# Kernel optimization log

Measured on AMD Instinct MI355X. Metric: run time of the kernel, lower is better.

## Reference

```python
import jax, jax.numpy as jnp
import numpy as np

HIDDEN = 64
EPS = 0.001


def _gru_cell(x, h, w_ih, w_hh, b_ih, b_hh):
    # PyTorch GRUCell math. w_ih: [3H, D], w_hh: [3H, H], gates ordered (r, z, n).
    gi = x @ w_ih.T + b_ih  # [B, 3H]
    gh = h @ w_hh.T + b_hh  # [B, 3H]
    i_r, i_z, i_n = jnp.split(gi, 3, axis=-1)
    h_r, h_z, h_n = jnp.split(gh, 3, axis=-1)
    r = jax.nn.sigmoid(i_r + h_r)
    z = jax.nn.sigmoid(i_z + h_z)
    n = jnp.tanh(i_n + r * h_n)
    return (1.0 - z) * n + z * h


def setup_inputs() -> dict:
    key = jax.random.key(0)
    ks = jax.random.split(key, 12)
    B, T, state_dim, action_dim = 2048, 512, 64, 8
    H = HIDDEN
    k_in = 1.0 / np.sqrt(H)  # PyTorch GRUCell init bound
    u = lambda k, shp: jax.random.uniform(k, shp, jnp.float32, -k_in, k_in)
    return {
        "state": jax.random.normal(ks[0], (B, T, state_dim), jnp.float32),
        "w_ih1": u(ks[1], (3 * H, state_dim)),
        "w_hh1": u(ks[2], (3 * H, H)),
        "b_ih1": u(ks[3], (3 * H,)),
        "b_hh1": u(ks[4], (3 * H,)),
        "w_ih2": u(ks[5], (3 * H, H)),
        "w_hh2": u(ks[6], (3 * H, H)),
        "b_ih2": u(ks[7], (3 * H,)),
        "b_hh2": u(ks[8], (3 * H,)),
        "fc_w": jax.random.uniform(ks[9], (action_dim, H), jnp.float32, -EPS, EPS),
        "fc_b": u(ks[10], (action_dim,)),
    }


def reference(state, w_ih1, w_hh1, b_ih1, b_hh1, w_ih2, w_hh2, b_ih2, b_hh2, fc_w, fc_b):
    B = state.shape[0]
    h0 = jnp.zeros((B, HIDDEN), state.dtype)

    def step(carry, x_t):
        s1, s2 = carry
        s1 = _gru_cell(x_t, s1, w_ih1, w_hh1, b_ih1, b_hh1)
        s2 = _gru_cell(s1, s2, w_ih2, w_hh2, b_ih2, b_hh2)
        return (s1, s2), None

    xs = jnp.swapaxes(state, 0, 1)  # [T, B, state_dim]
    (_, s2), _ = jax.lax.scan(step, (h0, h0), xs)
    return s2 @ fc_w.T + fc_b  # [B, action_dim]
```

## Files before the change

### kernel.cpp

```cpp
#include <hip/hip_runtime.h>

#define T_STEPS 512
#define HID 64
#define SPB 8
#define NT 512

typedef _Float16 f16x8 __attribute__((ext_vector_type(8)));
typedef float f32x4 __attribute__((ext_vector_type(4)));

#define MFMA(a, b, c) __builtin_amdgcn_mfma_f32_16x16x32_f16(a, b, c, 0, 0, 0)

#define LOG2E 1.44269504088896340736f

__device__ __forceinline__ unsigned pkh(float a, float b) {
    unsigned short ua = __builtin_bit_cast(unsigned short, (_Float16)a);
    unsigned short ub = __builtin_bit_cast(unsigned short, (_Float16)b);
    return (unsigned)ua | ((unsigned)ub << 16);
}
__device__ __forceinline__ float dpp_ror8(float x) {
    int i = __builtin_bit_cast(int, x);
    int r = __builtin_amdgcn_mov_dpp(i, 0x128, 0xF, 0xF, true);
    return __builtin_bit_cast(float, r);
}
__device__ __forceinline__ char* swz(const void* base, int s, int kbyte) {
    int off = s * 128 + kbyte;
    off ^= (s & 7) << 4;
    return (char*)base + off;
}
__device__ __forceinline__ f16x8 g8rowS(const float* __restrict__ p, float s) {
    f16x8 r;
#pragma unroll
    for (int j = 0; j < 8; ++j) r[j] = (_Float16)(p[j] * s);
    return r;
}

#define BAR() do { asm volatile("s_waitcnt lgkmcnt(0)" ::: "memory"); \
                   __builtin_amdgcn_s_barrier();                      \
                   asm volatile("" ::: "memory"); } while (0)

__global__ __launch_bounds__(NT, 1)
void gru2_pf2(const float* __restrict__ state,
              const float* __restrict__ w_ih1, const float* __restrict__ w_hh1,
              const float* __restrict__ b_ih1, const float* __restrict__ b_hh1,
              const float* __restrict__ w_ih2, const float* __restrict__ w_hh2,
              const float* __restrict__ b_ih2, const float* __restrict__ b_hh2,
              const float* __restrict__ fc_w,  const float* __restrict__ fc_b,
              float* __restrict__ out)
{
    __shared__ __align__(16) unsigned short xb[2][16][64];
    __shared__ __align__(16) unsigned short h1b[2][16][64];
    __shared__ __align__(16) unsigned short h2b[2][16][64];

    const int tid  = threadIdx.x;
    const int wv8  = tid >> 6;
    const bool isA = wv8 < 4;
    const int w    = wv8 & 3;
    const int lane = tid & 63;
    const int i16  = lane & 15;
    const int g    = lane >> 4;
    const int g8   = g * 8;
    const int b0   = blockIdx.x * SPB;
    const bool realc = (i16 < 8);

    const float* Wp = isA ? w_ih1 : w_ih2;
    const float* Wq = isA ? w_hh1 : w_hh2;
    const float* Bi = isA ? b_ih1 : b_ih2;
    const float* Bh = isA ? b_hh1 : b_hh2;

    const int rA = (16 * w + i16) * HID;
    const int zA = rA + 64 * HID;
    const int nA = rA + 128 * HID;
    f16x8 ar[4], az[4], ani[2], anh[2];
    ar[0]  = g8rowS(Wp + rA + g8, -LOG2E);  ar[1]  = g8rowS(Wp + rA + 32 + g8, -LOG2E);
    ar[2]  = g8rowS(Wq + rA + g8, -LOG2E);  ar[3]  = g8rowS(Wq + rA + 32 + g8, -LOG2E);
    az[0]  = g8rowS(Wp + zA + g8, -LOG2E);  az[1]  = g8rowS(Wp + zA + 32 + g8, -LOG2E);
    az[2]  = g8rowS(Wq + zA + g8, -LOG2E);  az[3]  = g8rowS(Wq + zA + 32 + g8, -LOG2E);
    ani[0] = g8rowS(Wp + nA + g8, 2.0f * LOG2E);
    ani[1] = g8rowS(Wp + nA + 32 + g8, 2.0f * LOG2E);
    anh[0] = g8rowS(Wq + nA + g8, 2.0f * LOG2E);
    anh[1] = g8rowS(Wq + nA + 32 + g8, 2.0f * LOG2E);

    f32x4 bR4, bZ4, bNi4, bNh4;
#pragma unroll
    for (int q = 0; q < 4; ++q) {
        const int r0 = 16 * w + 4 * g + q;
        bR4[q]  = -LOG2E * (Bi[r0] + Bh[r0]);
        bZ4[q]  = -LOG2E * (Bi[64 + r0] + Bh[64 + r0]);
        bNi4[q] = 2.0f * LOG2E * Bi[128 + r0];
        bNh4[q] = 2.0f * LOG2E * Bh[128 + r0];
    }

    char* rp[2][2]; char* rq[2][2]; char* wd[2]; char* sa[2];
    const int scol = i16 & 7;
    const int qb4  = realc ? 0 : 4;
#pragma unroll
    for (int c = 0; c < 2; ++c) {
        const void* Pb = isA ? (const void*)xb[c]      : (const void*)h1b[c ^ 1];
        const void* Qb = isA ? (const void*)h1b[c ^ 1] : (const void*)h2b[c];
        void* Db       = isA ? (void*)h1b[c]           : (void*)h2b[c ^ 1];
        rp[c][0] = swz(Pb, i16, 16 * g);
        rp[c][1] = swz(Pb, i16, 64 + 16 * g);
        rq[c][0] = swz(Qb, i16, 16 * g);
        rq[c][1] = swz(Qb, i16, 64 + 16 * g);
        wd[c]    = swz(Db, scol, 32 * w + 8 * g + qb4);
        sa[c]    = swz(xb[c ^ 1], (tid >> 5) & 7, (tid & 31) * 4);
    }

    for (int k = tid; k < 2 * 16 * 64; k += NT) {
        ((unsigned short*)xb)[k]  = 0;
        ((unsigned short*)h1b)[k] = 0;
        ((unsigned short*)h2b)[k] = 0;
    }
    __syncthreads();

    const int ss = (tid >> 5) & 7;
    const int sk = (tid & 31) * 2;
    const float* xgp = state + (size_t)(b0 + ss) * T_STEPS * HID + sk;
    float2 PFa = make_float2(0.0f, 0.0f);
    float2 PFb = make_float2(0.0f, 0.0f);
    if (tid < 256) {
        float2 v0 = *(const float2*)xgp;
        *(unsigned*)swz(xb[0], ss, sk * 2) = pkh(v0.x, v0.y);
        PFa = *(const float2*)(xgp + HID);
        PFb = *(const float2*)(xgp + 2 * HID);
    }
    const float* xnext = xgp + 3 * HID;
    __syncthreads();

    float hr0 = 0.0f, hr1 = 0.0f;
    f16x8 p0 = {}, p1 = {}, q0 = {}, q1 = {};

#define ITER(TT, CUR)                                                            \
  {                                                                              \
    const bool active = isA ? ((TT) < T_STEPS) : ((TT) >= 1);                    \
    if (active) {                                                                \
      if (realc) {       \
        p0 = *(const f16x8*)rp[CUR][0];                                          \
        p1 = *(const f16x8*)rp[CUR][1];                                          \
        q0 = *(const f16x8*)rq[CUR][0];                                          \
        q1 = *(const f16x8*)rq[CUR][1];                                          \
      }                                                                          \
      __builtin_amdgcn_s_setprio(1);                                             \
      f32x4 aR  = MFMA(ar[0], p0, bR4);                                          \
      f32x4 aZ  = MFMA(az[0], p0, bZ4);                                          \
      f32x4 aNi = MFMA(ani[0], p0, bNi4);                                        \
      f32x4 aNh = MFMA(anh[0], q0, bNh4);                                        \
      aR  = MFMA(ar[1], p1, aR);   aR  = MFMA(ar[2], q0, aR);                    \
      aR  = MFMA(ar[3], q1, aR);                                                 \
      aZ  = MFMA(az[1], p1, aZ);   aZ  = MFMA(az[2], q0, aZ);                    \
      aZ  = MFMA(az[3], q1, aZ);                                                 \
      aNi = MFMA(ani[1], p1, aNi);                                               \
      aNh = MFMA(anh[1], q1, aNh);                                               \
      __builtin_amdgcn_s_setprio(0);                                             \
        \
      float vR0  = realc ? aR[0]  : dpp_ror8(aR[2]);                             \
      float vR1  = realc ? aR[1]  : dpp_ror8(aR[3]);                             \
      float vZ0  = realc ? aZ[0]  : dpp_ror8(aZ[2]);                             \
      float vZ1  = realc ? aZ[1]  : dpp_ror8(aZ[3]);                             \
      float vNi0 = realc ? aNi[0] : dpp_ror8(aNi[2]);                            \
      float vNi1 = realc ? aNi[1] : dpp_ror8(aNi[3]);                            \
      float vNh0 = realc ? aNh[0] : dpp_ror8(aNh[2]);                            \
      float vNh1 = realc ? aNh[1] : dpp_ror8(aNh[3]);                            \
      {                                                                          \
        float rg0 = __builtin_amdgcn_rcpf(1.0f + __builtin_amdgcn_exp2f(vR0));   \
        float zg0 = __builtin_amdgcn_rcpf(1.0f + __builtin_amdgcn_exp2f(vZ0));   \
        float e20 = __builtin_amdgcn_exp2f(fmaf(rg0, vNh0, vNi0));               \
        float ng0 = fmaf(-2.0f, __builtin_amdgcn_rcpf(1.0f + e20), 1.0f);        \
        hr0 = fmaf(zg0, hr0 - ng0, ng0);                                         \
        float rg1 = __builtin_amdgcn_rcpf(1.0f + __builtin_amdgcn_exp2f(vR1));   \
        float zg1 = __builtin_amdgcn_rcpf(1.0f + __builtin_amdgcn_exp2f(vZ1));   \
        float e21 = __builtin_amdgcn_exp2f(fmaf(rg1, vNh1, vNi1));               \
        float ng1 = fmaf(-2.0f, __builtin_amdgcn_rcpf(1.0f + e21), 1.0f);        \
        hr1 = fmaf(zg1, hr1 - ng1, ng1);                                         \
      }                                                                          \
      *(unsigned*)wd[CUR] = pkh(hr0, hr1);                                       \
    }                                                                            \
    if (tid < 256 && (TT) < T_STEPS) {                                           \
      *(unsigned*)sa[CUR] = pkh(PFa.x, PFa.y);   \
      PFa = PFb;                                                                 \
      PFb = *(const float2*)xnext;                            \
      xnext += ((TT) <= T_STEPS - 5) ? HID : 0;                                  \
    }                                                                            \
    BAR();                                                                       \
  }

    for (int t = 0; t < T_STEPS; t += 2) {
        ITER(t, 0)
        ITER(t + 1, 1)
    }
    ITER(T_STEPS, 0)
#undef ITER

    if (tid < 64) {
        const int s = tid >> 3, a = tid & 7;
        float acc = fc_b[a];
#pragma unroll
        for (int j = 0; j < HID; ++j) {
            _Float16 hv = *(_Float16*)swz(h2b[1], s, j * 2);
            acc = fmaf((float)hv, fc_w[a * HID + j], acc);
        }
        out[(size_t)(b0 + s) * 8 + a] = acc;
    }
}

extern "C" void kernel_launch(void* const* d_in, const int* in_sizes, int n_in,
                              void* d_out, int out_size, void* d_ws, size_t ws_size,
                              hipStream_t stream) {
    (void)in_sizes; (void)n_in; (void)d_ws; (void)ws_size; (void)out_size;
    const float* state = (const float*)d_in[0];
    const float* w_ih1 = (const float*)d_in[1];
    const float* w_hh1 = (const float*)d_in[2];
    const float* b_ih1 = (const float*)d_in[3];
    const float* b_hh1 = (const float*)d_in[4];
    const float* w_ih2 = (const float*)d_in[5];
    const float* w_hh2 = (const float*)d_in[6];
    const float* b_ih2 = (const float*)d_in[7];
    const float* b_hh2 = (const float*)d_in[8];
    const float* fc_w  = (const float*)d_in[9];
    const float* fc_b  = (const float*)d_in[10];
    float* out = (float*)d_out;

    dim3 grid(2048 / SPB);
    dim3 block(NT);
    gru2_pf2<<<grid, block, 0, stream>>>(state,
                                         w_ih1, w_hh1, b_ih1, b_hh1,
                                         w_ih2, w_hh2, b_ih2, b_hh2,
                                         fc_w, fc_b, out);
}
```

Measured before the change: 242.3 us.

## Stagger GRU layer phases so MFMA and gate math of the two layers alternate

Splits each timestep into two barrier-separated halves. Layer-1 waves run their MFMAs while layer-2 waves run gate activations, and then the roles swap. The goal is to spread matrix-core and transcendental/VALU work evenly across the phases instead of having every wave contend for the same unit at once. In exchange it doubles the barriers per step and changes the h2 double-buffer indexing, so correctness depends on the new buffer parity and lag.

```diff
diff --git a/kernel.cpp b/kernel.cpp
--- a/kernel.cpp
+++ b/kernel.cpp
@@ -38,14 +38,59 @@
                    __builtin_amdgcn_s_barrier();                      \
                    asm volatile("" ::: "memory"); } while (0)
 
+#define GATES_WRITE(CUR)                                                       \
+  {                                                                            \
+    float vR0  = realc ? aR[0]  : dpp_ror8(aR[2]);                             \
+    float vR1  = realc ? aR[1]  : dpp_ror8(aR[3]);                             \
+    float vZ0  = realc ? aZ[0]  : dpp_ror8(aZ[2]);                             \
+    float vZ1  = realc ? aZ[1]  : dpp_ror8(aZ[3]);                             \
+    float vNi0 = realc ? aNi[0] : dpp_ror8(aNi[2]);                            \
+    float vNi1 = realc ? aNi[1] : dpp_ror8(aNi[3]);                            \
+    float vNh0 = realc ? aNh[0] : dpp_ror8(aNh[2]);                            \
+    float vNh1 = realc ? aNh[1] : dpp_ror8(aNh[3]);                            \
+    float rg0 = __builtin_amdgcn_rcpf(1.0f + __builtin_amdgcn_exp2f(vR0));     \
+    float zg0 = __builtin_amdgcn_rcpf(1.0f + __builtin_amdgcn_exp2f(vZ0));     \
+    float e20 = __builtin_amdgcn_exp2f(fmaf(rg0, vNh0, vNi0));                 \
+    float ng0 = fmaf(-2.0f, __builtin_amdgcn_rcpf(1.0f + e20), 1.0f);          \
+    hr0 = fmaf(zg0, hr0 - ng0, ng0);                                           \
+    float rg1 = __builtin_amdgcn_rcpf(1.0f + __builtin_amdgcn_exp2f(vR1));     \
+    float zg1 = __builtin_amdgcn_rcpf(1.0f + __builtin_amdgcn_exp2f(vZ1));     \
+    float e21 = __builtin_amdgcn_exp2f(fmaf(rg1, vNh1, vNi1));                 \
+    float ng1 = fmaf(-2.0f, __builtin_amdgcn_rcpf(1.0f + e21), 1.0f);          \
+    hr1 = fmaf(zg1, hr1 - ng1, ng1);                                           \
+    *(unsigned*)wd[CUR] = pkh(hr0, hr1);                                       \
+  }
+
+#define READ_MFMA(CUR)                                                         \
+  {                                                                            \
+    if (realc) {                                                               \
+      p0 = *(const f16x8*)rp[CUR][0];                                          \
+      p1 = *(const f16x8*)rp[CUR][1];                                          \
+      q0 = *(const f16x8*)rq[CUR][0];                                          \
+      q1 = *(const f16x8*)rq[CUR][1];                                          \
+    }                                                                          \
+    __builtin_amdgcn_s_setprio(1);                                             \
+    aR  = MFMA(ar[0], p0, bR4);                                                \
+    aZ  = MFMA(az[0], p0, bZ4);                                                \
+    aNi = MFMA(ani[0], p0, bNi4);                                              \
+    aNh = MFMA(anh[0], q0, bNh4);                                              \
+    aR  = MFMA(ar[1], p1, aR);   aR  = MFMA(ar[2], q0, aR);                    \
+    aR  = MFMA(ar[3], q1, aR);                                                 \
+    aZ  = MFMA(az[1], p1, aZ);   aZ  = MFMA(az[2], q0, aZ);                    \
+    aZ  = MFMA(az[3], q1, aZ);                                                 \
+    aNi = MFMA(ani[1], p1, aNi);                                               \
+    aNh = MFMA(anh[1], q1, aNh);                                               \
+    __builtin_amdgcn_s_setprio(0);                                             \
+  }
+
 __global__ __launch_bounds__(NT, 1)
-void gru2_pf2(const float* __restrict__ state,
-              const float* __restrict__ w_ih1, const float* __restrict__ w_hh1,
-              const float* __restrict__ b_ih1, const float* __restrict__ b_hh1,
-              const float* __restrict__ w_ih2, const float* __restrict__ w_hh2,
-              const float* __restrict__ b_ih2, const float* __restrict__ b_hh2,
-              const float* __restrict__ fc_w,  const float* __restrict__ fc_b,
-              float* __restrict__ out)
+void gru2_stag(const float* __restrict__ state,
+               const float* __restrict__ w_ih1, const float* __restrict__ w_hh1,
+               const float* __restrict__ b_ih1, const float* __restrict__ b_hh1,
+               const float* __restrict__ w_ih2, const float* __restrict__ w_hh2,
+               const float* __restrict__ b_ih2, const float* __restrict__ b_hh2,
+               const float* __restrict__ fc_w,  const float* __restrict__ fc_b,
+               float* __restrict__ out)
 {
     __shared__ __align__(16) unsigned short xb[2][16][64];
     __shared__ __align__(16) unsigned short h1b[2][16][64];
@@ -97,7 +142,7 @@
     for (int c = 0; c < 2; ++c) {
         const void* Pb = isA ? (const void*)xb[c]      : (const void*)h1b[c ^ 1];
         const void* Qb = isA ? (const void*)h1b[c ^ 1] : (const void*)h2b[c];
-        void* Db       = isA ? (void*)h1b[c]           : (void*)h2b[c ^ 1];
+        void* Db       = isA ? (void*)h1b[c]           : (void*)h2b[c];
         rp[c][0] = swz(Pb, i16, 16 * g);
         rp[c][1] = swz(Pb, i16, 64 + 16 * g);
         rq[c][0] = swz(Qb, i16, 16 * g);
@@ -128,68 +173,36 @@
     __syncthreads();
 
     float hr0 = 0.0f, hr1 = 0.0f;
+    f32x4 aR = {0,0,0,0}, aZ = {0,0,0,0}, aNi = {0,0,0,0}, aNh = {0,0,0,0};
     f16x8 p0 = {}, p1 = {}, q0 = {}, q1 = {};
 
-#define ITER(TT, CUR)                                                            \
-  {                                                                              \
-    const bool active = isA ? ((TT) < T_STEPS) : ((TT) >= 1);                    \
-    if (active) {                                                                \
-      if (realc) {       \
-        p0 = *(const f16x8*)rp[CUR][0];                                          \
-        p1 = *(const f16x8*)rp[CUR][1];                                          \
-        q0 = *(const f16x8*)rq[CUR][0];                                          \
-        q1 = *(const f16x8*)rq[CUR][1];                                          \
-      }                                                                          \
-      __builtin_amdgcn_s_setprio(1);                                             \
-      f32x4 aR  = MFMA(ar[0], p0, bR4);                                          \
-      f32x4 aZ  = MFMA(az[0], p0, bZ4);                                          \
-      f32x4 aNi = MFMA(ani[0], p0, bNi4);                                        \
-      f32x4 aNh = MFMA(anh[0], q0, bNh4);                                        \
-      aR  = MFMA(ar[1], p1, aR);   aR  = MFMA(ar[2], q0, aR);                    \
-      aR  = MFMA(ar[3], q1, aR);                                                 \
-      aZ  = MFMA(az[1], p1, aZ);   aZ  = MFMA(az[2], q0, aZ);                    \
-      aZ  = MFMA(az[3], q1, aZ);                                                 \
-      aNi = MFMA(ani[1], p1, aNi);                                               \
-      aNh = MFMA(anh[1], q1, aNh);                                               \
-      __builtin_amdgcn_s_setprio(0);                                             \
-        \
-      float vR0  = realc ? aR[0]  : dpp_ror8(aR[2]);                             \
-      float vR1  = realc ? aR[1]  : dpp_ror8(aR[3]);                             \
-      float vZ0  = realc ? aZ[0]  : dpp_ror8(aZ[2]);                             \
-      float vZ1  = realc ? aZ[1]  : dpp_ror8(aZ[3]);                             \
-      float vNi0 = realc ? aNi[0] : dpp_ror8(aNi[2]);                            \
-      float vNi1 = realc ? aNi[1] : dpp_ror8(aNi[3]);                            \
-      float vNh0 = realc ? aNh[0] : dpp_ror8(aNh[2]);                            \
-      float vNh1 = realc ? aNh[1] : dpp_ror8(aNh[3]);                            \
-      {                                                                          \
-        float rg0 = __builtin_amdgcn_rcpf(1.0f + __builtin_amdgcn_exp2f(vR0));   \
-        float zg0 = __builtin_amdgcn_rcpf(1.0f + __builtin_amdgcn_exp2f(vZ0));   \
-        float e20 = __builtin_amdgcn_exp2f(fmaf(rg0, vNh0, vNi0));               \
-        float ng0 = fmaf(-2.0f, __builtin_amdgcn_rcpf(1.0f + e20), 1.0f);        \
-        hr0 = fmaf(zg0, hr0 - ng0, ng0);                                         \
-        float rg1 = __builtin_amdgcn_rcpf(1.0f + __builtin_amdgcn_exp2f(vR1));   \
-        float zg1 = __builtin_amdgcn_rcpf(1.0f + __builtin_amdgcn_exp2f(vZ1));   \
-        float e21 = __builtin_amdgcn_exp2f(fmaf(rg1, vNh1, vNi1));               \
-        float ng1 = fmaf(-2.0f, __builtin_amdgcn_rcpf(1.0f + e21), 1.0f);        \
-        hr1 = fmaf(zg1, hr1 - ng1, ng1);                                         \
-      }                                                                          \
-      *(unsigned*)wd[CUR] = pkh(hr0, hr1);                                       \
-    }                                                                            \
-    if (tid < 256 && (TT) < T_STEPS) {                                           \
-      *(unsigned*)sa[CUR] = pkh(PFa.x, PFa.y);   \
-      PFa = PFb;                                                                 \
-      PFb = *(const float2*)xnext;                            \
-      xnext += ((TT) <= T_STEPS - 5) ? HID : 0;                                  \
-    }                                                                            \
-    BAR();                                                                       \
+#define STEP(TT, CUR)                                                          \
+  {                                                                            \
+    if (isA) {                                                                 \
+      if ((TT) < T_STEPS) {                                                    \
+        READ_MFMA(CUR)                                                         \
+        *(unsigned*)sa[CUR] = pkh(PFa.x, PFa.y);            \
+        PFa = PFb;                                                             \
+        PFb = *(const float2*)xnext;                                           \
+        xnext += ((TT) <= T_STEPS - 5) ? HID : 0;                              \
+      }                                                                        \
+    } else {                                                                   \
+      if ((TT) >= 2) GATES_WRITE(CUR)          \
+    }                                                                          \
+    BAR();                                                                     \
+    if (isA) {                                                                 \
+      if ((TT) < T_STEPS) GATES_WRITE(CUR)       \
+    } else {                                                                   \
+      if ((TT) >= 1 && (TT) <= T_STEPS) READ_MFMA(CUR)  \
+    }                                                                          \
+    BAR();                                                                     \
   }
 
-    for (int t = 0; t < T_STEPS; t += 2) {
-        ITER(t, 0)
-        ITER(t + 1, 1)
-    }
-    ITER(T_STEPS, 0)
-#undef ITER
+    for (int t = 0; t < T_STEPS + 2; t += 2) {
+        STEP(t, 0)
+        STEP(t + 1, 1)
+    }
+#undef STEP
 
     if (tid < 64) {
         const int s = tid >> 3, a = tid & 7;
@@ -222,8 +235,8 @@
 
     dim3 grid(2048 / SPB);
     dim3 block(NT);
-    gru2_pf2<<<grid, block, 0, stream>>>(state,
-                                         w_ih1, w_hh1, b_ih1, b_hh1,
-                                         w_ih2, w_hh2, b_ih2, b_hh2,
-                                         fc_w, fc_b, out);
-}
+    gru2_stag<<<grid, block, 0, stream>>>(state,
+                                          w_ih1, w_hh1, b_ih1, b_hh1,
+                                          w_ih2, w_hh2, b_ih2, b_hh2,
+                                          fc_w, fc_b, out);
+}
```

Measured after the change: 425.8 us. 75.7% more time.
